# Optimization experiments

Measured on AMD Instinct MI355X. Metric: run time of the kernel, lower is better.

## Reference

```python
import jax, jax.numpy as jnp
import numpy as np

HEADS = 16
EPS = 1e-6

def _rmsnorm(x, g):
    # x: (..., d); norm = ||x||_2 * d^-0.5 (matches torch.norm-based RMSNorm)
    d = x.shape[-1]
    nrm = jnp.linalg.norm(x, axis=-1, keepdims=True) * (d ** -0.5)
    return x / (nrm + EPS) * g

def _rope(x, cos, sin):
    # x: (b,n,h,d) -> complex pairs over last dim; cos/sin: (1,n,1,d//2)
    b, n, h, d = x.shape
    xr = x.reshape(b, n, h, d // 2, 2)
    re, im = xr[..., 0], xr[..., 1]
    out_re = re * cos - im * sin
    out_im = re * sin + im * cos
    return jnp.stack([out_re, out_im], axis=-1).reshape(b, n, h, d)

def setup_inputs() -> dict:
    key = jax.random.key(0)
    ks = jax.random.split(key, 8)
    b, n, dim = 4, 4096, 1024
    d = dim // HEADS
    x = jax.random.normal(ks[0], (b, n, dim), dtype=jnp.float32)
    # rope freqs as cos/sin of random angles (broadcast shape 1,n,1,d//2)
    ang = jax.random.uniform(ks[1], (1, n, 1, d // 2), dtype=jnp.float32) * (2 * np.pi)
    freqs_cos = jnp.cos(ang)
    freqs_sin = jnp.sin(ang)
    sc = dim ** -0.5
    w_qkv = jax.random.normal(ks[2], (dim, 3 * dim), dtype=jnp.float32) * sc
    g_q = jnp.ones((d,), dtype=jnp.float32)
    g_k = jnp.ones((d,), dtype=jnp.float32)
    w_proj = jax.random.normal(ks[3], (dim, dim), dtype=jnp.float32) * sc
    b_proj = jnp.zeros((dim,), dtype=jnp.float32)
    return {"x": x, "freqs_cos": freqs_cos, "freqs_sin": freqs_sin,
            "w_qkv": w_qkv, "g_q": g_q, "g_k": g_k,
            "w_proj": w_proj, "b_proj": b_proj}

def reference(x, freqs_cos, freqs_sin, w_qkv, g_q, g_k, w_proj, b_proj):
    b, n, dim = x.shape
    h = HEADS
    d = dim // h
    scale = d ** -0.5
    qkv = x @ w_qkv  # (b,n,3*dim)
    q, k, v = jnp.split(qkv, 3, axis=-1)
    q = q.reshape(b, n, h, d)
    k = k.reshape(b, n, h, d)
    v = v.reshape(b, n, h, d)
    q = _rmsnorm(q, g_q)
    k = _rmsnorm(k, g_k)
    q = _rope(q, freqs_cos, freqs_sin)
    k = _rope(k, freqs_cos, freqs_sin)
    # per-token head-mixing attention: (b,n,h,h)
    attn = jnp.einsum('bnhd,bngd->bnhg', q, k) * scale
    attn = jax.nn.softmax(attn, axis=-1)
    out = jnp.einsum('bnhg,bngd->bnhd', attn, v).reshape(b, n, dim)
    return out @ w_proj + b_proj
```

## Files before the change

### kernel.cpp

```cpp
#include <hip/hip_runtime.h>
#include <hip/hip_bf16.h>
#include <stddef.h>

#define NTOK   16384
#define SEQN   4096
#define DIM    1024
#define K3     3072
#define HEADS  16
#define HD     64

typedef __attribute__((ext_vector_type(8)))  short  short8;
typedef __attribute__((ext_vector_type(4)))  float  float4v;

static __device__ __forceinline__ unsigned short f32_to_bf16_bits(float f) {
    unsigned u = __float_as_uint(f);
    unsigned r = u + 0x7fffu + ((u >> 16) & 1u);
    return (unsigned short)(r >> 16);
}
static __device__ __forceinline__ unsigned pack_bf16x2(float lo, float hi) {
    return (unsigned)f32_to_bf16_bits(lo) | ((unsigned)f32_to_bf16_bits(hi) << 16);
}
static __device__ __forceinline__ void unpack_bf16x8(uint4 u, float* f) {
    f[0] = __uint_as_float(u.x << 16); f[1] = __uint_as_float(u.x & 0xffff0000u);
    f[2] = __uint_as_float(u.y << 16); f[3] = __uint_as_float(u.y & 0xffff0000u);
    f[4] = __uint_as_float(u.z << 16); f[5] = __uint_as_float(u.z & 0xffff0000u);
    f[6] = __uint_as_float(u.w << 16); f[7] = __uint_as_float(u.w & 0xffff0000u);
}

typedef const void __attribute__((address_space(1)))* gas_ptr;
typedef void __attribute__((address_space(3)))* las_ptr;
static __device__ __forceinline__ void gload_lds16(const unsigned short* g,
                                                   unsigned short* l) {
    __builtin_amdgcn_global_load_lds((gas_ptr)g, (las_ptr)l, 16, 0, 0);
}

__global__ void cvt_f32_bf16(const float4* __restrict__ in,
                             ushort4* __restrict__ out, int n4) {
    int i = blockIdx.x * blockDim.x + threadIdx.x;
    if (i < n4) {
        float4 v = in[i];
        ushort4 o;
        o.x = f32_to_bf16_bits(v.x);
        o.y = f32_to_bf16_bits(v.y);
        o.z = f32_to_bf16_bits(v.z);
        o.w = f32_to_bf16_bits(v.w);
        out[i] = o;
    }
}

__global__ void transpose_cvt(const float* __restrict__ in,
                              unsigned short* __restrict__ out,
                              int K, int N) {
    __shared__ float t[32][33];
    int n0 = blockIdx.x * 32, k0 = blockIdx.y * 32;
    int tx = threadIdx.x, ty = threadIdx.y;
    #pragma unroll
    for (int r = ty; r < 32; r += 8)
        t[r][tx] = in[(size_t)(k0 + r) * N + n0 + tx];
    __syncthreads();
    #pragma unroll
    for (int r = ty; r < 32; r += 8)
        out[(size_t)(n0 + r) * K + k0 + tx] = f32_to_bf16_bits(t[tx][r]);
}

template<int WITH_BIAS>
__global__ __launch_bounds__(512, 2) void gemm_bf16_256(
    const unsigned short* __restrict__ A,
    const unsigned short* __restrict__ Bt,
    void* __restrict__ Cout,
    const float* __restrict__ bias,
    int M, int N)
{
    constexpr int K = 1024;
    __shared__ unsigned short As[2][256][64];
    __shared__ unsigned short Bs[2][256][64];

    const int tid  = threadIdx.x;
    const int wave = tid >> 6;
    const int lane = tid & 63;
    const int wm   = wave >> 2;
    const int wn   = wave & 3;
    const int l15  = lane & 15;
    const int l4   = lane >> 4;
    const int l7   = lane & 7;

    const int nwg = (int)gridDim.x;
    const int bid = (int)blockIdx.x;
    const int swz = (bid & 7) * (nwg >> 3) + (bid >> 3);
    const int ntn = N >> 8;
    const int rowBase = (swz / ntn) << 8;
    const int colBase = (swz % ntn) << 8;
    (void)M;

    const int drow = lane >> 3;
    const int lc   = l7 ^ drow;
    const unsigned short* gA = A  + (size_t)(rowBase + drow) * K + lc * 8;
    const unsigned short* gB = Bt + (size_t)(colBase + drow) * K + lc * 8;

    float4v acc[8][4];
    #pragma unroll
    for (int m = 0; m < 8; m++)
        #pragma unroll
        for (int n = 0; n < 4; n++) acc[m][n] = (float4v)0.0f;

    short8 aF[4][2], b0F[2][2], b1F[2][2];

#define STG_A(f, oddH, T) do {                                               \
    const int ra_ = ((wave >> 2) * 128) + (oddH) * 64 + (wave & 3) * 16;     \
    gload_lds16(gA + (size_t)(ra_    ) * K + (size_t)(T) * 64, &As[f][ra_    ][0]); \
    gload_lds16(gA + (size_t)(ra_ + 8) * K + (size_t)(T) * 64, &As[f][ra_ + 8][0]); \
  } while (0)
#define STG_B(f, oddH, T) do {                                               \
    const int rb_ = ((wave >> 1) * 64) + (oddH) * 32 + (wave & 1) * 16;      \
    gload_lds16(gB + (size_t)(rb_    ) * K + (size_t)(T) * 64, &Bs[f][rb_    ][0]); \
    gload_lds16(gB + (size_t)(rb_ + 8) * K + (size_t)(T) * 64, &Bs[f][rb_ + 8][0]); \
  } while (0)

#define RD_A(f, a) do {                                                      \
    _Pragma("unroll")                                                        \
    for (int ra = 0; ra < 4; ra++) {                                         \
      const unsigned short* r_ = &As[f][wm * 128 + (a) * 64 + ra * 16 + l15][0]; \
      aF[ra][0] = *(const short8*)(r_ + (((    l4) ^ l7) * 8));              \
      aF[ra][1] = *(const short8*)(r_ + (((4 + l4) ^ l7) * 8));              \
    } } while (0)
#define RD_B(f, b, dst) do {                                                 \
    _Pragma("unroll")                                                        \
    for (int cb = 0; cb < 2; cb++) {                                         \
      const unsigned short* r_ = &Bs[f][wn * 64 + (b) * 32 + cb * 16 + l15][0]; \
      dst[cb][0] = *(const short8*)(r_ + (((    l4) ^ l7) * 8));             \
      dst[cb][1] = *(const short8*)(r_ + (((4 + l4) ^ l7) * 8));             \
    } } while (0)

#define MM(a, b, bF) do {                                                    \
    _Pragma("unroll")                                                        \
    for (int ra = 0; ra < 4; ra++)                                           \
      _Pragma("unroll")                                                      \
      for (int cb = 0; cb < 2; cb++) {                                       \
        acc[(a)*4+ra][(b)*2+cb] = __builtin_amdgcn_mfma_f32_16x16x32_bf16(   \
            aF[ra][0], bF[cb][0], acc[(a)*4+ra][(b)*2+cb], 0, 0, 0);         \
        acc[(a)*4+ra][(b)*2+cb] = __builtin_amdgcn_mfma_f32_16x16x32_bf16(   \
            aF[ra][1], bF[cb][1], acc[(a)*4+ra][(b)*2+cb], 0, 0, 0);         \
      } } while (0)

#define BAR()   __builtin_amdgcn_s_barrier()
#define SB()    __builtin_amdgcn_sched_barrier(0)
#define VM(n)   asm volatile("s_waitcnt vmcnt(" #n ")" ::: "memory")
#define P1()    __builtin_amdgcn_s_setprio(1)
#define P0()    __builtin_amdgcn_s_setprio(0)

    STG_A(0,0,0); STG_B(0,0,0); STG_B(0,1,0); STG_A(0,1,0);
    STG_A(1,0,1); STG_B(1,0,1); STG_B(1,1,1); STG_A(1,1,1);
    VM(8);
    BAR();
    RD_A(0,0); RD_B(0,0,b0F);
    SB(); BAR();

    #pragma unroll 1
    for (int i = 0; i < 7; i++) {
        const int T0 = 2 * i + 2, T1 = 2 * i + 3;
        RD_B(0,1,b1F);                 STG_A(0,0,T0);
        P1(); MM(0,0,b0F); P0(); SB(); BAR();
        P1(); MM(0,1,b1F); P0(); RD_A(0,1);  STG_B(0,0,T0); SB(); BAR();
        P1(); MM(1,1,b1F); P0();             STG_B(0,1,T0); SB(); BAR();
        P1(); MM(1,0,b0F); P0(); VM(6);
        RD_A(1,0); RD_B(1,0,b0F);            STG_A(0,1,T0); SB(); BAR();
        RD_B(1,1,b1F);                 STG_A(1,0,T1);
        P1(); MM(0,0,b0F); P0(); SB(); BAR();
        P1(); MM(0,1,b1F); P0(); RD_A(1,1);  STG_B(1,0,T1); SB(); BAR();
        P1(); MM(1,1,b1F); P0();             STG_B(1,1,T1); SB(); BAR();
        P1(); MM(1,0,b0F); P0(); VM(6);
        RD_A(0,0); RD_B(0,0,b0F);            STG_A(1,1,T1); SB(); BAR();
    }

    RD_B(0,1,b1F);
    P1(); MM(0,0,b0F); P0(); SB(); BAR();
    P1(); MM(0,1,b1F); P0(); RD_A(0,1); SB(); BAR();
    P1(); MM(1,1,b1F); P0(); SB(); BAR();
    P1(); MM(1,0,b0F); P0(); VM(0); SB(); BAR();
    RD_A(1,0); RD_B(1,0,b0F);
    RD_B(1,1,b1F);
    P1(); MM(0,0,b0F); P0();
    P1(); MM(0,1,b1F); P0(); RD_A(1,1);
    P1(); MM(1,1,b1F); P0();
    P1(); MM(1,0,b0F); P0();

    #pragma unroll
    for (int m = 0; m < 8; m++) {
        const int row = rowBase + wm * 128 + m * 16 + l4 * 4;
        #pragma unroll
        for (int n = 0; n < 4; n++) {
            const int col = colBase + wn * 64 + n * 16 + l15;
            if (WITH_BIAS) {
                const float bv = bias[col];
                #pragma unroll
                for (int r = 0; r < 4; r++)
                    ((float*)Cout)[(size_t)(row + r) * N + col] = acc[m][n][r] + bv;
            } else {
                #pragma unroll
                for (int r = 0; r < 4; r++)
                    ((unsigned short*)Cout)[(size_t)(row + r) * N + col] =
                        f32_to_bf16_bits(acc[m][n][r]);
            }
        }
    }
#undef STG_A
#undef STG_B
#undef RD_A
#undef RD_B
#undef MM
#undef BAR
#undef SB
#undef VM
#undef P1
#undef P0
}

__global__ __launch_bounds__(256) void attn_tok(
    const unsigned short* __restrict__ qkv,
    const float* __restrict__ fcos,
    const float* __restrict__ fsin,
    const float* __restrict__ gq,
    const float* __restrict__ gk,
    unsigned short* __restrict__ outb)
{
    __shared__ float kl[4][16][68];
    __shared__ float vl[4][16][68];

    const int tid  = threadIdx.x;
    const int wv   = tid >> 6;
    const int lane = tid & 63;
    const int h    = lane & 15;
    const int p    = lane >> 4;
    const int tok  = blockIdx.x * 4 + wv;
    const int n    = tok & (SEQN - 1);

    const unsigned short* base = qkv + (size_t)tok * K3 + h * 64 + p * 16;
    uint4 qr0 = *(const uint4*)(base);
    uint4 qr1 = *(const uint4*)(base + 8);
    uint4 kr0 = *(const uint4*)(base + DIM);
    uint4 kr1 = *(const uint4*)(base + DIM + 8);
    uint4 vr0 = *(const uint4*)(base + 2 * DIM);
    uint4 vr1 = *(const uint4*)(base + 2 * DIM + 8);

    float q[16], k[16], v[16];
    unpack_bf16x8(qr0, q); unpack_bf16x8(qr1, q + 8);
    unpack_bf16x8(kr0, k); unpack_bf16x8(kr1, k + 8);
    unpack_bf16x8(vr0, v); unpack_bf16x8(vr1, v + 8);

    float ssq = 0.f, ssk = 0.f;
    #pragma unroll
    for (int i = 0; i < 16; i++) { ssq += q[i] * q[i]; ssk += k[i] * k[i]; }
    ssq += __shfl_xor(ssq, 16); ssq += __shfl_xor(ssq, 32);
    ssk += __shfl_xor(ssk, 16); ssk += __shfl_xor(ssk, 32);
    const float sq = 1.0f / (sqrtf(ssq) * 0.125f + 1e-6f);
    const float sk = 1.0f / (sqrtf(ssk) * 0.125f + 1e-6f);

    #pragma unroll
    for (int c = 0; c < 4; c++) {
        float4 gg = *(const float4*)(gq + p * 16 + c * 4);
        float4 gh = *(const float4*)(gk + p * 16 + c * 4);
        q[c*4+0] *= sq * gg.x; q[c*4+1] *= sq * gg.y;
        q[c*4+2] *= sq * gg.z; q[c*4+3] *= sq * gg.w;
        k[c*4+0] *= sk * gh.x; k[c*4+1] *= sk * gh.y;
        k[c*4+2] *= sk * gh.z; k[c*4+3] *= sk * gh.w;
    }

    {
        const float* cb = fcos + n * 32 + p * 8;
        const float* sb = fsin + n * 32 + p * 8;
        float4 c0 = *(const float4*)cb, c1 = *(const float4*)(cb + 4);
        float4 s0 = *(const float4*)sb, s1 = *(const float4*)(sb + 4);
        float cs[8] = {c0.x,c0.y,c0.z,c0.w,c1.x,c1.y,c1.z,c1.w};
        float sn[8] = {s0.x,s0.y,s0.z,s0.w,s1.x,s1.y,s1.z,s1.w};
        #pragma unroll
        for (int j = 0; j < 8; j++) {
            float re = q[2*j], im = q[2*j+1];
            q[2*j]   = re * cs[j] - im * sn[j];
            q[2*j+1] = re * sn[j] + im * cs[j];
            re = k[2*j]; im = k[2*j+1];
            k[2*j]   = re * cs[j] - im * sn[j];
            k[2*j+1] = re * sn[j] + im * cs[j];
        }
    }

    {
        float* krow = &kl[wv][h][p * 16];
        float* vrow = &vl[wv][h][p * 16];
        #pragma unroll
        for (int c = 0; c < 4; c++) {
            *(float4*)(krow + c*4) = make_float4(k[c*4], k[c*4+1], k[c*4+2], k[c*4+3]);
            *(float4*)(vrow + c*4) = make_float4(v[c*4], v[c*4+1], v[c*4+2], v[c*4+3]);
        }
    }

    float s[16];
    #pragma unroll
    for (int g = 0; g < 16; g++) {
        const float* kg = &kl[wv][g][p * 16];
        float4 a0 = *(const float4*)(kg);
        float4 a1 = *(const float4*)(kg + 4);
        float4 a2 = *(const float4*)(kg + 8);
        float4 a3 = *(const float4*)(kg + 12);
        s[g] = q[0]*a0.x + q[1]*a0.y + q[2]*a0.z + q[3]*a0.w
             + q[4]*a1.x + q[5]*a1.y + q[6]*a1.z + q[7]*a1.w
             + q[8]*a2.x + q[9]*a2.y + q[10]*a2.z + q[11]*a2.w
             + q[12]*a3.x + q[13]*a3.y + q[14]*a3.z + q[15]*a3.w;
    }
    #pragma unroll
    for (int g = 0; g < 16; g++) {
        s[g] += __shfl_xor(s[g], 16);
        s[g] += __shfl_xor(s[g], 32);
        s[g] *= 0.125f;
    }

    float m = s[0];
    #pragma unroll
    for (int g = 1; g < 16; g++) m = fmaxf(m, s[g]);
    float sum = 0.f;
    #pragma unroll
    for (int g = 0; g < 16; g++) { s[g] = __expf(s[g] - m); sum += s[g]; }
    const float inv = 1.0f / sum;

    float o[16];
    #pragma unroll
    for (int i = 0; i < 16; i++) o[i] = 0.f;
    #pragma unroll
    for (int g = 0; g < 16; g++) {
        const float pg = s[g] * inv;
        const float* vg = &vl[wv][g][p * 16];
        float4 b0 = *(const float4*)(vg);
        float4 b1 = *(const float4*)(vg + 4);
        float4 b2 = *(const float4*)(vg + 8);
        float4 b3 = *(const float4*)(vg + 12);
        o[0]  += pg * b0.x; o[1]  += pg * b0.y; o[2]  += pg * b0.z; o[3]  += pg * b0.w;
        o[4]  += pg * b1.x; o[5]  += pg * b1.y; o[6]  += pg * b1.z; o[7]  += pg * b1.w;
        o[8]  += pg * b2.x; o[9]  += pg * b2.y; o[10] += pg * b2.z; o[11] += pg * b2.w;
        o[12] += pg * b3.x; o[13] += pg * b3.y; o[14] += pg * b3.z; o[15] += pg * b3.w;
    }

    uint4 r0, r1;
    r0.x = pack_bf16x2(o[0],  o[1]);  r0.y = pack_bf16x2(o[2],  o[3]);
    r0.z = pack_bf16x2(o[4],  o[5]);  r0.w = pack_bf16x2(o[6],  o[7]);
    r1.x = pack_bf16x2(o[8],  o[9]);  r1.y = pack_bf16x2(o[10], o[11]);
    r1.z = pack_bf16x2(o[12], o[13]); r1.w = pack_bf16x2(o[14], o[15]);
    unsigned short* ob = outb + (size_t)tok * DIM + h * 64 + p * 16;
    *(uint4*)(ob)     = r0;
    *(uint4*)(ob + 8) = r1;
}

extern "C" void kernel_launch(void* const* d_in, const int* in_sizes, int n_in,
                              void* d_out, int out_size, void* d_ws, size_t ws_size,
                              hipStream_t stream) {
    const float* x      = (const float*)d_in[0];
    const float* fcos   = (const float*)d_in[1];
    const float* fsin   = (const float*)d_in[2];
    const float* w_qkv  = (const float*)d_in[3];
    const float* g_q    = (const float*)d_in[4];
    const float* g_k    = (const float*)d_in[5];
    const float* w_proj = (const float*)d_in[6];
    const float* b_proj = (const float*)d_in[7];
    float* out = (float*)d_out;

    char* ws = (char*)d_ws;
    unsigned short* xb      = (unsigned short*)(ws);
    unsigned short* wqkvT   = (unsigned short*)(ws + 33554432);
    unsigned short* wprojT  = (unsigned short*)(ws + 39845888);
    unsigned short* qkv     = (unsigned short*)(ws + 41943040);
    unsigned short* attnout = (unsigned short*)(ws + 142606336);
    (void)ws_size; (void)in_sizes; (void)n_in; (void)out_size;

    {
        int n4 = (NTOK * DIM) / 4;
        cvt_f32_bf16<<<(n4 + 255) / 256, 256, 0, stream>>>(
            (const float4*)x, (ushort4*)xb, n4);
        transpose_cvt<<<dim3(K3 / 32, DIM / 32), dim3(32, 8), 0, stream>>>(
            w_qkv, wqkvT, DIM, K3);
        transpose_cvt<<<dim3(DIM / 32, DIM / 32), dim3(32, 8), 0, stream>>>(
            w_proj, wprojT, DIM, DIM);
    }
    gemm_bf16_256<0><<<dim3((NTOK / 256) * (K3 / 256)), 512, 0, stream>>>(
        xb, wqkvT, (void*)qkv, nullptr, NTOK, K3);
    attn_tok<<<NTOK / 4, 256, 0, stream>>>(qkv, fcos, fsin, g_q, g_k, attnout);
    gemm_bf16_256<1><<<dim3((NTOK / 256) * (DIM / 256)), 512, 0, stream>>>(
        attnout, wprojT, (void*)out, b_proj, NTOK, DIM);
}
```

Measured before the change: 330.2 us.

## Compute per-token head-mixing attention with bf16 MFMA instead of FP32 LDS dot products

Rewrites the per-token attention kernel to compute QK^T and PV with 16x16x32 bf16 MFMA instructions instead of scalar FP32 dot products through shared memory. Precision in the score matmul is kept with a split hi/lo bf16 decomposition of q and k. Softmax probabilities are redistributed across lanes with shuffles to form the A operand. V is gathered directly from global memory with strided 2-byte loads, and the output is written with scattered 2-byte stores. This removes LDS traffic and FP32 FMA work but adds uncoalesced loads and stores and bf16 rounding of the probabilities.

```diff
diff --git a/kernel.cpp b/kernel.cpp
--- a/kernel.cpp
+++ b/kernel.cpp
@@ -25,6 +25,14 @@
     f[2] = __uint_as_float(u.y << 16); f[3] = __uint_as_float(u.y & 0xffff0000u);
     f[4] = __uint_as_float(u.z << 16); f[5] = __uint_as_float(u.z & 0xffff0000u);
     f[6] = __uint_as_float(u.w << 16); f[7] = __uint_as_float(u.w & 0xffff0000u);
+}
+static __device__ __forceinline__ short8 pack8(const float* f) {
+    uint4 u;
+    u.x = pack_bf16x2(f[0], f[1]);
+    u.y = pack_bf16x2(f[2], f[3]);
+    u.z = pack_bf16x2(f[4], f[5]);
+    u.w = pack_bf16x2(f[6], f[7]);
+    return __builtin_bit_cast(short8, u);
 }
 
 typedef const void __attribute__((address_space(1)))* gas_ptr;
@@ -215,7 +223,7 @@
 #undef P0
 }
 
-__global__ __launch_bounds__(256) void attn_tok(
+__global__ __launch_bounds__(256) void attn_tok_mfma(
     const unsigned short* __restrict__ qkv,
     const float* __restrict__ fcos,
     const float* __restrict__ fsin,
@@ -223,9 +231,6 @@
     const float* __restrict__ gk,
     unsigned short* __restrict__ outb)
 {
-    __shared__ float kl[4][16][68];
-    __shared__ float vl[4][16][68];
-
     const int tid  = threadIdx.x;
     const int wv   = tid >> 6;
     const int lane = tid & 63;
@@ -234,18 +239,15 @@
     const int tok  = blockIdx.x * 4 + wv;
     const int n    = tok & (SEQN - 1);
 
-    const unsigned short* base = qkv + (size_t)tok * K3 + h * 64 + p * 16;
-    uint4 qr0 = *(const uint4*)(base);
-    uint4 qr1 = *(const uint4*)(base + 8);
-    uint4 kr0 = *(const uint4*)(base + DIM);
-    uint4 kr1 = *(const uint4*)(base + DIM + 8);
-    uint4 vr0 = *(const uint4*)(base + 2 * DIM);
-    uint4 vr1 = *(const uint4*)(base + 2 * DIM + 8);
-
-    float q[16], k[16], v[16];
-    unpack_bf16x8(qr0, q); unpack_bf16x8(qr1, q + 8);
-    unpack_bf16x8(kr0, k); unpack_bf16x8(kr1, k + 8);
-    unpack_bf16x8(vr0, v); unpack_bf16x8(vr1, v + 8);
+    const unsigned short* base = qkv + (size_t)tok * K3 + h * 64 + p * 8;
+    uint4 qlo = *(const uint4*)(base);
+    uint4 qhi = *(const uint4*)(base + 32);
+    uint4 klo = *(const uint4*)(base + DIM);
+    uint4 khi = *(const uint4*)(base + DIM + 32);
+
+    float q[16], k[16];
+    unpack_bf16x8(qlo, q); unpack_bf16x8(qhi, q + 8);
+    unpack_bf16x8(klo, k); unpack_bf16x8(khi, k + 8);
 
     float ssq = 0.f, ssk = 0.f;
     #pragma unroll
@@ -255,97 +257,112 @@
     const float sq = 1.0f / (sqrtf(ssq) * 0.125f + 1e-6f);
     const float sk = 1.0f / (sqrtf(ssk) * 0.125f + 1e-6f);
 
-    #pragma unroll
-    for (int c = 0; c < 4; c++) {
-        float4 gg = *(const float4*)(gq + p * 16 + c * 4);
-        float4 gh = *(const float4*)(gk + p * 16 + c * 4);
-        q[c*4+0] *= sq * gg.x; q[c*4+1] *= sq * gg.y;
-        q[c*4+2] *= sq * gg.z; q[c*4+3] *= sq * gg.w;
-        k[c*4+0] *= sk * gh.x; k[c*4+1] *= sk * gh.y;
-        k[c*4+2] *= sk * gh.z; k[c*4+3] *= sk * gh.w;
-    }
-
     {
-        const float* cb = fcos + n * 32 + p * 8;
-        const float* sb = fsin + n * 32 + p * 8;
-        float4 c0 = *(const float4*)cb, c1 = *(const float4*)(cb + 4);
-        float4 s0 = *(const float4*)sb, s1 = *(const float4*)(sb + 4);
-        float cs[8] = {c0.x,c0.y,c0.z,c0.w,c1.x,c1.y,c1.z,c1.w};
-        float sn[8] = {s0.x,s0.y,s0.z,s0.w,s1.x,s1.y,s1.z,s1.w};
+        float4 g0 = *(const float4*)(gq + p * 8);
+        float4 g1 = *(const float4*)(gq + p * 8 + 4);
+        float4 g2 = *(const float4*)(gq + 32 + p * 8);
+        float4 g3 = *(const float4*)(gq + 32 + p * 8 + 4);
+        float4 h0 = *(const float4*)(gk + p * 8);
+        float4 h1 = *(const float4*)(gk + p * 8 + 4);
+        float4 h2 = *(const float4*)(gk + 32 + p * 8);
+        float4 h3 = *(const float4*)(gk + 32 + p * 8 + 4);
+        float gg[16] = {g0.x,g0.y,g0.z,g0.w, g1.x,g1.y,g1.z,g1.w,
+                        g2.x,g2.y,g2.z,g2.w, g3.x,g3.y,g3.z,g3.w};
+        float hh[16] = {h0.x,h0.y,h0.z,h0.w, h1.x,h1.y,h1.z,h1.w,
+                        h2.x,h2.y,h2.z,h2.w, h3.x,h3.y,h3.z,h3.w};
+        #pragma unroll
+        for (int i = 0; i < 16; i++) { q[i] *= sq * gg[i]; k[i] *= sk * hh[i]; }
+    }
+
+    {
+        float4 c0 = *(const float4*)(fcos + n * 32 + p * 4);
+        float4 c1 = *(const float4*)(fcos + n * 32 + 16 + p * 4);
+        float4 s0 = *(const float4*)(fsin + n * 32 + p * 4);
+        float4 s1 = *(const float4*)(fsin + n * 32 + 16 + p * 4);
+        float cs[8] = {c0.x,c0.y,c0.z,c0.w, c1.x,c1.y,c1.z,c1.w};
+        float sn[8] = {s0.x,s0.y,s0.z,s0.w, s1.x,s1.y,s1.z,s1.w};
         #pragma unroll
         for (int j = 0; j < 8; j++) {
-            float re = q[2*j], im = q[2*j+1];
-            q[2*j]   = re * cs[j] - im * sn[j];
-            q[2*j+1] = re * sn[j] + im * cs[j];
-            re = k[2*j]; im = k[2*j+1];
-            k[2*j]   = re * cs[j] - im * sn[j];
-            k[2*j+1] = re * sn[j] + im * cs[j];
+            const int lo = (j < 4) ? 2*j : 8 + 2*(j-4);
+            float re = q[lo], im = q[lo+1];
+            q[lo]   = re * cs[j] - im * sn[j];
+            q[lo+1] = re * sn[j] + im * cs[j];
+            re = k[lo]; im = k[lo+1];
+            k[lo]   = re * cs[j] - im * sn[j];
+            k[lo+1] = re * sn[j] + im * cs[j];
         }
     }
 
-    {
-        float* krow = &kl[wv][h][p * 16];
-        float* vrow = &vl[wv][h][p * 16];
-        #pragma unroll
-        for (int c = 0; c < 4; c++) {
-            *(float4*)(krow + c*4) = make_float4(k[c*4], k[c*4+1], k[c*4+2], k[c*4+3]);
-            *(float4*)(vrow + c*4) = make_float4(v[c*4], v[c*4+1], v[c*4+2], v[c*4+3]);
-        }
-    }
-
-    float s[16];
-    #pragma unroll
-    for (int g = 0; g < 16; g++) {
-        const float* kg = &kl[wv][g][p * 16];
-        float4 a0 = *(const float4*)(kg);
-        float4 a1 = *(const float4*)(kg + 4);
-        float4 a2 = *(const float4*)(kg + 8);
-        float4 a3 = *(const float4*)(kg + 12);
-        s[g] = q[0]*a0.x + q[1]*a0.y + q[2]*a0.z + q[3]*a0.w
-             + q[4]*a1.x + q[5]*a1.y + q[6]*a1.z + q[7]*a1.w
-             + q[8]*a2.x + q[9]*a2.y + q[10]*a2.z + q[11]*a2.w
-             + q[12]*a3.x + q[13]*a3.y + q[14]*a3.z + q[15]*a3.w;
-    }
-    #pragma unroll
-    for (int g = 0; g < 16; g++) {
-        s[g] += __shfl_xor(s[g], 16);
-        s[g] += __shfl_xor(s[g], 32);
-        s[g] *= 0.125f;
-    }
-
-    float m = s[0];
-    #pragma unroll
-    for (int g = 1; g < 16; g++) m = fmaxf(m, s[g]);
-    float sum = 0.f;
-    #pragma unroll
-    for (int g = 0; g < 16; g++) { s[g] = __expf(s[g] - m); sum += s[g]; }
-    const float inv = 1.0f / sum;
-
-    float o[16];
-    #pragma unroll
-    for (int i = 0; i < 16; i++) o[i] = 0.f;
-    #pragma unroll
-    for (int g = 0; g < 16; g++) {
-        const float pg = s[g] * inv;
-        const float* vg = &vl[wv][g][p * 16];
-        float4 b0 = *(const float4*)(vg);
-        float4 b1 = *(const float4*)(vg + 4);
-        float4 b2 = *(const float4*)(vg + 8);
-        float4 b3 = *(const float4*)(vg + 12);
-        o[0]  += pg * b0.x; o[1]  += pg * b0.y; o[2]  += pg * b0.z; o[3]  += pg * b0.w;
-        o[4]  += pg * b1.x; o[5]  += pg * b1.y; o[6]  += pg * b1.z; o[7]  += pg * b1.w;
-        o[8]  += pg * b2.x; o[9]  += pg * b2.y; o[10] += pg * b2.z; o[11] += pg * b2.w;
-        o[12] += pg * b3.x; o[13] += pg * b3.y; o[14] += pg * b3.z; o[15] += pg * b3.w;
-    }
-
-    uint4 r0, r1;
-    r0.x = pack_bf16x2(o[0],  o[1]);  r0.y = pack_bf16x2(o[2],  o[3]);
-    r0.z = pack_bf16x2(o[4],  o[5]);  r0.w = pack_bf16x2(o[6],  o[7]);
-    r1.x = pack_bf16x2(o[8],  o[9]);  r1.y = pack_bf16x2(o[10], o[11]);
-    r1.z = pack_bf16x2(o[12], o[13]); r1.w = pack_bf16x2(o[14], o[15]);
-    unsigned short* ob = outb + (size_t)tok * DIM + h * 64 + p * 16;
-    *(uint4*)(ob)     = r0;
-    *(uint4*)(ob + 8) = r1;
+    #pragma unroll
+    for (int i = 0; i < 16; i++) q[i] *= 0.125f;
+
+    float qr[16], kr[16];
+    #pragma unroll
+    for (int i = 0; i < 16; i++) {
+        qr[i] = q[i] - __uint_as_float((unsigned)f32_to_bf16_bits(q[i]) << 16);
+        kr[i] = k[i] - __uint_as_float((unsigned)f32_to_bf16_bits(k[i]) << 16);
+    }
+    short8 qH0 = pack8(q),  qH1 = pack8(q + 8);
+    short8 qL0 = pack8(qr), qL1 = pack8(qr + 8);
+    short8 kH0 = pack8(k),  kH1 = pack8(k + 8);
+    short8 kL0 = pack8(kr), kL1 = pack8(kr + 8);
+
+    float4v st = (float4v)0.0f;
+    st = __builtin_amdgcn_mfma_f32_16x16x32_bf16(kH0, qH0, st, 0, 0, 0);
+    st = __builtin_amdgcn_mfma_f32_16x16x32_bf16(kH1, qH1, st, 0, 0, 0);
+    st = __builtin_amdgcn_mfma_f32_16x16x32_bf16(kH0, qL0, st, 0, 0, 0);
+    st = __builtin_amdgcn_mfma_f32_16x16x32_bf16(kH1, qL1, st, 0, 0, 0);
+    st = __builtin_amdgcn_mfma_f32_16x16x32_bf16(kL0, qH0, st, 0, 0, 0);
+    st = __builtin_amdgcn_mfma_f32_16x16x32_bf16(kL1, qH1, st, 0, 0, 0);
+
+    float m = fmaxf(fmaxf(st[0], st[1]), fmaxf(st[2], st[3]));
+    m = fmaxf(m, __shfl_xor(m, 16));
+    m = fmaxf(m, __shfl_xor(m, 32));
+    float e0 = __expf(st[0] - m), e1 = __expf(st[1] - m);
+    float e2 = __expf(st[2] - m), e3 = __expf(st[3] - m);
+    float sum = e0 + e1 + e2 + e3;
+    sum += __shfl_xor(sum, 16); sum += __shfl_xor(sum, 32);
+    const float hinv = 0.5f / sum;
+
+    const unsigned pe01 = pack_bf16x2(e0 * hinv, e1 * hinv);
+    const unsigned pe23 = pack_bf16x2(e2 * hinv, e3 * hinv);
+    const int ph   = p & 1;
+    const int src0 = h + 32 * ph;
+    const int src1 = src0 + 16;
+    uint4 pu;
+    pu.x = (unsigned)__shfl((int)pe01, src0);
+    pu.y = (unsigned)__shfl((int)pe23, src0);
+    pu.z = (unsigned)__shfl((int)pe01, src1);
+    pu.w = (unsigned)__shfl((int)pe23, src1);
+    const short8 paF = __builtin_bit_cast(short8, pu);
+
+    const unsigned short* vb = qkv + (size_t)tok * K3 + 2 * DIM
+                             + (size_t)(ph * 8) * 64 + h;
+    short8 bvf[4];
+    #pragma unroll
+    for (int db = 0; db < 4; db++) {
+        const unsigned short* vd = vb + db * 16;
+        uint4 w;
+        w.x = (unsigned)vd[0 * 64] | ((unsigned)vd[1 * 64] << 16);
+        w.y = (unsigned)vd[2 * 64] | ((unsigned)vd[3 * 64] << 16);
+        w.z = (unsigned)vd[4 * 64] | ((unsigned)vd[5 * 64] << 16);
+        w.w = (unsigned)vd[6 * 64] | ((unsigned)vd[7 * 64] << 16);
+        bvf[db] = __builtin_bit_cast(short8, w);
+    }
+
+    float4v o0 = __builtin_amdgcn_mfma_f32_16x16x32_bf16(paF, bvf[0], (float4v)0.0f, 0, 0, 0);
+    float4v o1 = __builtin_amdgcn_mfma_f32_16x16x32_bf16(paF, bvf[1], (float4v)0.0f, 0, 0, 0);
+    float4v o2 = __builtin_amdgcn_mfma_f32_16x16x32_bf16(paF, bvf[2], (float4v)0.0f, 0, 0, 0);
+    float4v o3 = __builtin_amdgcn_mfma_f32_16x16x32_bf16(paF, bvf[3], (float4v)0.0f, 0, 0, 0);
+
+    unsigned short* ob = outb + (size_t)tok * DIM + (size_t)(p * 4) * 64 + h;
+    #pragma unroll
+    for (int r = 0; r < 4; r++) {
+        ob[(size_t)r * 64 +  0] = f32_to_bf16_bits(o0[r]);
+        ob[(size_t)r * 64 + 16] = f32_to_bf16_bits(o1[r]);
+        ob[(size_t)r * 64 + 32] = f32_to_bf16_bits(o2[r]);
+        ob[(size_t)r * 64 + 48] = f32_to_bf16_bits(o3[r]);
+    }
 }
 
 extern "C" void kernel_launch(void* const* d_in, const int* in_sizes, int n_in,
@@ -380,7 +397,7 @@
     }
     gemm_bf16_256<0><<<dim3((NTOK / 256) * (K3 / 256)), 512, 0, stream>>>(
         xb, wqkvT, (void*)qkv, nullptr, NTOK, K3);
-    attn_tok<<<NTOK / 4, 256, 0, stream>>>(qkv, fcos, fsin, g_q, g_k, attnout);
+    attn_tok_mfma<<<NTOK / 4, 256, 0, stream>>>(qkv, fcos, fsin, g_q, g_k, attnout);
     gemm_bf16_256<1><<<dim3((NTOK / 256) * (DIM / 256)), 512, 0, stream>>>(
         attnout, wprojT, (void*)out, b_proj, NTOK, DIM);
 }
```

Result: faster. 318.6 us (-3.5%).
